# Optimization experiments

Hardware: AMD Instinct MI355X
Metric: run time of the kernel (lower is better)

## Reference

```python
import jax, jax.numpy as jnp
import numpy as np

KH, KW = 3, 3
PAD = 1
STRIDE = 1


def dht1(x):
    # 1D Discrete Hartley Transform along last axis: Re(FFT) - Im(FFT)
    f = jnp.fft.fft(x, axis=-1)
    return f.real - f.imag


def dht2(x, fft_h, fft_w):
    # zero-pad trailing two dims up to (fft_h, fft_w), then DHT along w then h
    pad_h = fft_h - x.shape[-2]
    pad_w = fft_w - x.shape[-1]
    pads = [(0, 0)] * (x.ndim - 2) + [(0, pad_h), (0, pad_w)]
    x = jnp.pad(x, pads)
    x = dht1(x)
    x = jnp.swapaxes(dht1(jnp.swapaxes(x, -1, -2)), -1, -2)
    return x


def setup_inputs() -> dict:
    key = jax.random.key(0)
    k1, k2 = jax.random.split(key)
    x = jax.random.normal(k1, (8, 64, 128, 128), dtype=jnp.float32)
    weight = jax.random.normal(k2, (64, 64, KH, KW), dtype=jnp.float32)
    return {"x": x, "weight": weight}


def reference(x, weight):
    b, c_in, h, w = x.shape
    out_h = (h + 2 * PAD - KH) // STRIDE + 1
    out_w = (w + 2 * PAD - KW) // STRIDE + 1
    x_p = jnp.pad(x, ((0, 0), (0, 0), (PAD, PAD), (PAD, PAD)))
    fft_h = h + 2 * PAD + KH - 1
    fft_w = w + 2 * PAD + KW - 1

    x_ht = dht2(x_p, fft_h, fft_w)          # [B, Cin, fh, fw]
    w_ht = dht2(weight, fft_h, fft_w)        # [Cout, Cin, fh, fw]

    x_f = jnp.flip(x_ht, axis=(-2, -1))
    w_f = jnp.flip(w_ht, axis=(-2, -1))

    # Fused combine + sum over Cin: avoids [B,Cout,Cin,fh,fw] intermediates.
    t1 = jnp.einsum('bchw,ochw->bohw', x_ht, w_ht)
    t2 = jnp.einsum('bchw,ochw->bohw', x_ht, w_f)
    t3 = jnp.einsum('bchw,ochw->bohw', x_f, w_ht)
    t4 = jnp.einsum('bchw,ochw->bohw', x_f, w_f)
    out_ht = (t1 + t2 + t3 - t4) * 0.5

    # idht2 in the source applies only the 1/n scaling twice (no transform)
    output = out_ht / jnp.asarray(fft_h * fft_w, dtype=out_ht.dtype)
    return output[:, :, :out_h, :out_w]
```

## Files before the change

kernel.cpp:

```cpp
#include <hip/hip_runtime.h>
#include <hip/hip_fp16.h>


#define SCALE (0.5f / 17424.0f)
#define MFMA  __builtin_amdgcn_mfma_f32_16x16x32_f16

typedef __attribute__((ext_vector_type(8))) _Float16 f16x8;
typedef __attribute__((ext_vector_type(4))) _Float16 f16x4;
typedef __attribute__((ext_vector_type(4))) float    f32x4;

__global__ __launch_bounds__(256) void build_all(
    const float* __restrict__ w, _Float16* __restrict__ Tf,
    _Float16* __restrict__ cfT, _Float16* __restrict__ hgT)
{
    const int bid = blockIdx.x;
    const int tid = threadIdx.x;
    const float step = 6.28318530717958647692f / 132.0f;
    if (bid < 144) {
        if (tid < 128) {
            float val = 0.f;
            if (bid < 132) {
                const int m = (bid * (tid + 1)) % 132;
                float s, c;
                sincosf((float)m * step, &s, &c);
                val = c + s;
            }
            Tf[bid * 128 + tid] = (_Float16)val;
        }
        return;
    }
    if (bid == 144) {
        if (tid < 128) {
            const int v = tid;
            float s, c;
            _Float16 o[8];
            o[0] = (_Float16)1.0f; o[3] = (_Float16)1.0f;
            o[6] = (_Float16)0.0f; o[7] = (_Float16)0.0f;
            sincosf((float)((v * 1) % 132) * step, &s, &c);       o[1] = (_Float16)(c + s);
            sincosf((float)((v * 2) % 132) * step, &s, &c);       o[2] = (_Float16)(c + s);
            sincosf((float)(((v + 1) * 1) % 132) * step, &s, &c); o[4] = (_Float16)(c - s);
            sincosf((float)(((v + 1) * 2) % 132) * step, &s, &c); o[5] = (_Float16)(c - s);
            *(f16x8*)(cfT + v * 8) = *(f16x8*)o;
        }
        return;
    }
    const int bid2 = bid - 145;
    const int u = bid2 >> 2;
    const int itbase = (bid2 & 3) * 4;
    float a[3], ap[3];
    a[0] = 1.f; ap[0] = 1.f;
    #pragma unroll
    for (int i = 1; i < 3; ++i) {
        float s, c;
        sincosf((float)((u * i) % 132) * step, &s, &c);
        a[i] = c + s;
        sincosf((float)(((u + 1) * i) % 132) * step, &s, &c);
        ap[i] = c - s;
    }
    for (int it = itbase; it < itbase + 4; ++it) {
        const int oc = it * 256 + tid;
        const float* wp = w + (size_t)oc * 9;
        float w9[9];
        #pragma unroll
        for (int q = 0; q < 9; ++q) w9[q] = wp[q];
        #pragma unroll
        for (int j = 0; j < 3; ++j) {
            const float h = a[0]*w9[j] + a[1]*w9[3+j] + a[2]*w9[6+j];
            const float g = ap[0]*w9[j] + ap[1]*w9[3+j] + ap[2]*w9[6+j];
            hgT[((size_t)u * 6 + j)     * 4096 + oc] = (_Float16)h;
            hgT[((size_t)u * 6 + 3 + j) * 4096 + oc] = (_Float16)g;
        }
    }
}

__global__ __launch_bounds__(512, 4) void dht2_fused(
    const float* __restrict__ x, const _Float16* __restrict__ Tf,
    _Float16* __restrict__ X)
{
    const int bc = blockIdx.x;
    const int tid = threadIdx.x, wv = tid >> 6, lane = tid & 63;
    const int col = lane & 15, quad = lane >> 4;
    __shared__ _Float16 Tfl[144][136];
    __shared__ _Float16 Y1l[144][136];

    const float* xp = x + (size_t)bc * 16384;
    const int ic = wv * 16 + col;

    float4 xv[4][2];
    #pragma unroll
    for (int kc = 0; kc < 4; ++kc) {
        const int k0 = kc * 32 + quad * 8;
        xv[kc][0] = *(const float4*)(xp + ic * 128 + k0);
        xv[kc][1] = *(const float4*)(xp + ic * 128 + k0 + 4);
    }
    #pragma unroll
    for (int s = 0; s < 5; ++s) {
        const int idx = tid + 512 * s;
        if (idx < 2304) {
            const int row = idx >> 4;
            const int ce  = (idx & 15) * 8;
            *(f16x8*)&Tfl[row][ce] = *(const f16x8*)(Tf + (size_t)idx * 8);
        }
    }
    f16x8 bfA[4];
    #pragma unroll
    for (int kc = 0; kc < 4; ++kc) {
        f16x8 t;
        t[0] = (_Float16)xv[kc][0].x; t[1] = (_Float16)xv[kc][0].y;
        t[2] = (_Float16)xv[kc][0].z; t[3] = (_Float16)xv[kc][0].w;
        t[4] = (_Float16)xv[kc][1].x; t[5] = (_Float16)xv[kc][1].y;
        t[6] = (_Float16)xv[kc][1].z; t[7] = (_Float16)xv[kc][1].w;
        bfA[kc] = t;
    }
    __syncthreads();

    f32x4 accA[9];
    #pragma unroll
    for (int mt = 0; mt < 9; ++mt) accA[mt] = (f32x4)0.f;
    #pragma unroll
    for (int kc = 0; kc < 4; ++kc) {
        const int k0 = kc * 32 + quad * 8;
        #pragma unroll
        for (int mt = 0; mt < 9; ++mt) {
            const f16x8 af = *(const f16x8*)&Tfl[mt * 16 + col][k0];
            accA[mt] = MFMA(af, bfA[kc], accA[mt], 0, 0, 0);
        }
    }
    #pragma unroll
    for (int mt = 0; mt < 9; ++mt)
        #pragma unroll
        for (int r = 0; r < 4; ++r)
            Y1l[mt * 16 + quad * 4 + r][ic] = (_Float16)accA[mt][r];
    __syncthreads();

    f32x4 accB[9];
    #pragma unroll
    for (int mt = 0; mt < 9; ++mt) accB[mt] = (f32x4)0.f;
    #pragma unroll
    for (int kc = 0; kc < 4; ++kc) {
        const int k0 = kc * 32 + quad * 8;
        const f16x8 bf = *(const f16x8*)&Y1l[wv * 16 + col][k0];
        #pragma unroll
        for (int mt = 0; mt < 9; ++mt) {
            const f16x8 af = *(const f16x8*)&Tfl[mt * 16 + col][k0];
            accB[mt] = MFMA(af, bf, accB[mt], 0, 0, 0);
        }
    }
    f32x4 accT[3];
    #pragma unroll
    for (int j = 0; j < 3; ++j) accT[j] = (f32x4)0.f;
    if (wv < 4) {
        #pragma unroll
        for (int kc = 0; kc < 4; ++kc) {
            const int k0 = kc * 32 + quad * 8;
            const f16x8 bf = *(const f16x8*)&Y1l[128 + col][k0];
            #pragma unroll
            for (int j = 0; j < 3; ++j) {
                if (j < 2 || wv == 0) {
                    const int mt = (j == 2) ? 8 : (wv * 2 + j);
                    const f16x8 af = *(const f16x8*)&Tfl[mt * 16 + col][k0];
                    accT[j] = MFMA(af, bf, accT[j], 0, 0, 0);
                }
            }
        }
    }
    __syncthreads();

    #pragma unroll
    for (int mt = 0; mt < 9; ++mt)
        #pragma unroll
        for (int r = 0; r < 4; ++r)
            Tfl[mt * 16 + quad * 4 + r][wv * 16 + col] = (_Float16)accB[mt][r];
    if (wv < 4 && col < 4) {
        #pragma unroll
        for (int j = 0; j < 3; ++j) {
            if (j < 2 || wv == 0) {
                const int mt = (j == 2) ? 8 : (wv * 2 + j);
                #pragma unroll
                for (int r = 0; r < 4; ++r)
                    Tfl[mt * 16 + quad * 4 + r][128 + col] = (_Float16)accT[j][r];
            }
        }
    }
    __syncthreads();
    _Float16* Xp = X + (size_t)bc * 17952;
    #pragma unroll
    for (int s = 0; s < 5; ++s) {
        const int ch = tid + 512 * s;
        if (ch < 2244) {
            const int u = ch / 17, kk = ch - u * 17;
            *(f16x8*)(Xp + u * 136 + kk * 8) = *(const f16x8*)&Tfl[u][kk * 8];
        }
    }
}

__global__ __launch_bounds__(512, 2) void combine_mfma(
    const _Float16* __restrict__ X, const _Float16* __restrict__ hgT,
    const _Float16* __restrict__ cfT, float* __restrict__ out)
{
    const int uidx = blockIdx.x;
    const int tid = threadIdx.x;
    const int wv8 = tid >> 6;
    const int half = wv8 >> 2;
    const int wv = wv8 & 3;
    const int lane = tid & 63;
    const int col = lane & 15, quad = lane >> 4;
    const int b = blockIdx.y * 2 + half;
    const int u2 = 131 - uidx;
    const bool doB = (uidx >= 4);

    __shared__ _Float16 Ps[2][132][72];
    __shared__ _Float16 Ms[2][132][72];

    {
        const int th = tid & 255;
        const int c = th >> 2, sub = th & 3;
        const _Float16* rowd = X + (size_t)(b * 64 + c) * 17952 + (size_t)uidx * 136;
        const _Float16* rowm = X + (size_t)(b * 64 + c) * 17952 + (size_t)u2 * 136;
        #pragma unroll
        for (int k = 0; k < 8; ++k) {
            const int v0 = sub * 32 + 4 * k;
            const f16x4 d = *(const f16x4*)(rowd + v0);
            const f16x4 m = *(const f16x4*)(rowm + (128 - v0));
            #pragma unroll
            for (int i = 0; i < 4; ++i) {
                Ps[half][v0 + i][c] = d[i] + m[3 - i];
                Ms[half][v0 + i][c] = d[i] - m[3 - i];
            }
        }
        if (sub == 0) {
            const f16x4 d = *(const f16x4*)(rowd + 128);
            const f16x4 m = *(const f16x4*)(rowm);
            #pragma unroll
            for (int i = 0; i < 4; ++i) {
                Ps[half][128 + i][c] = d[i] + m[3 - i];
                Ms[half][128 + i][c] = d[i] - m[3 - i];
            }
        }
    }

    const _Float16* hgu = hgT + (size_t)uidx * 6 * 4096;
    const int orow = wv * 16 + col;
    f16x8 hA[3][2], gA[3][2];
    #pragma unroll
    for (int kt = 0; kt < 3; ++kt)
        #pragma unroll
        for (int hf = 0; hf < 2; ++hf) {
            hA[kt][hf] = *(const f16x8*)(hgu + ((size_t)kt * 64 + orow) * 64 + hf * 32 + quad * 8);
            gA[kt][hf] = *(const f16x8*)(hgu + ((size_t)(3 + kt) * 64 + orow) * 64 + hf * 32 + quad * 8);
        }
    __syncthreads();

    float* outA = out + (((size_t)(b * 64 + wv * 16 + quad * 4)) * 128 + uidx) * 128 + col;
    float* outB = out + (((size_t)(b * 64 + wv * 16 + quad * 4)) * 128 + u2) * 128 + col;

    #pragma unroll
    for (int nt = 0; nt < 8; ++nt) {
        const int vA = nt * 16 + col;
        const int vB = 131 - vA;
        const f16x8 cf8 = *(const f16x8*)(cfT + (size_t)(nt * 16 + col) * 8);
        const float c1 = (float)cf8[1], c2 = (float)cf8[2];
        const float d1 = (float)cf8[4], d2 = (float)cf8[5];
        {
            const f16x8 p0 = *(const f16x8*)&Ps[half][vA][quad * 8];
            const f16x8 p1 = *(const f16x8*)&Ps[half][vA][32 + quad * 8];
            const f16x8 m0 = *(const f16x8*)&Ms[half][vA][quad * 8];
            const f16x8 m1 = *(const f16x8*)&Ms[half][vA][32 + quad * 8];
            f32x4 aP0 = (f32x4)0.f, aP1 = (f32x4)0.f, aP2 = (f32x4)0.f;
            f32x4 aM0 = (f32x4)0.f, aM1 = (f32x4)0.f, aM2 = (f32x4)0.f;
            aP0 = MFMA(hA[0][0], p0, aP0, 0, 0, 0); aP0 = MFMA(hA[0][1], p1, aP0, 0, 0, 0);
            aP1 = MFMA(hA[1][0], p0, aP1, 0, 0, 0); aP1 = MFMA(hA[1][1], p1, aP1, 0, 0, 0);
            aP2 = MFMA(hA[2][0], p0, aP2, 0, 0, 0); aP2 = MFMA(hA[2][1], p1, aP2, 0, 0, 0);
            aM0 = MFMA(gA[0][0], m0, aM0, 0, 0, 0); aM0 = MFMA(gA[0][1], m1, aM0, 0, 0, 0);
            aM1 = MFMA(gA[1][0], m0, aM1, 0, 0, 0); aM1 = MFMA(gA[1][1], m1, aM1, 0, 0, 0);
            aM2 = MFMA(gA[2][0], m0, aM2, 0, 0, 0); aM2 = MFMA(gA[2][1], m1, aM2, 0, 0, 0);
            #pragma unroll
            for (int r = 0; r < 4; ++r)
                outA[(size_t)r * 16384 + nt * 16] =
                    ((aP0[r] + c1 * aP1[r] + c2 * aP2[r]) +
                     (aM0[r] + d1 * aM1[r] + d2 * aM2[r])) * SCALE;
        }
        if (doB) {
            const f16x8 p0 = *(const f16x8*)&Ps[half][vB][quad * 8];
            const f16x8 p1 = *(const f16x8*)&Ps[half][vB][32 + quad * 8];
            const f16x8 m0 = *(const f16x8*)&Ms[half][vB][quad * 8];
            const f16x8 m1 = *(const f16x8*)&Ms[half][vB][32 + quad * 8];
            f32x4 bP0 = (f32x4)0.f, bP1 = (f32x4)0.f, bP2 = (f32x4)0.f;
            f32x4 bM0 = (f32x4)0.f, bM1 = (f32x4)0.f, bM2 = (f32x4)0.f;
            bP0 = MFMA(gA[0][0], p0, bP0, 0, 0, 0); bP0 = MFMA(gA[0][1], p1, bP0, 0, 0, 0);
            bP1 = MFMA(gA[1][0], p0, bP1, 0, 0, 0); bP1 = MFMA(gA[1][1], p1, bP1, 0, 0, 0);
            bP2 = MFMA(gA[2][0], p0, bP2, 0, 0, 0); bP2 = MFMA(gA[2][1], p1, bP2, 0, 0, 0);
            bM0 = MFMA(hA[0][0], m0, bM0, 0, 0, 0); bM0 = MFMA(hA[0][1], m1, bM0, 0, 0, 0);
            bM1 = MFMA(hA[1][0], m0, bM1, 0, 0, 0); bM1 = MFMA(hA[1][1], m1, bM1, 0, 0, 0);
            bM2 = MFMA(hA[2][0], m0, bM2, 0, 0, 0); bM2 = MFMA(hA[2][1], m1, bM2, 0, 0, 0);
            #pragma unroll
            for (int r = 0; r < 4; ++r)
                outB[(size_t)r * 16384 + nt * 16] =
                    ((bP0[r] + c1 * bP1[r] + c2 * bP2[r]) -
                     (bM0[r] + d1 * bM1[r] + d2 * bM2[r])) * SCALE;
        }
    }
}

extern "C" void kernel_launch(void* const* d_in, const int* in_sizes, int n_in,
                              void* d_out, int out_size, void* d_ws, size_t ws_size,
                              hipStream_t stream)
{
    const float* x = (const float*)d_in[0];
    const float* w = (const float*)d_in[1];
    char* ws = (char*)d_ws;
    _Float16* Tf  = (_Float16*)(ws);
    _Float16* cfT = (_Float16*)(ws + 36864);
    _Float16* X   = (_Float16*)(ws + 65536);
    _Float16* hgT = (_Float16*)(ws + 18448384);

    build_all<<<dim3(409), dim3(256), 0, stream>>>(w, Tf, cfT, hgT);

    dht2_fused<<<dim3(512), dim3(512), 0, stream>>>(x, Tf, X);

    combine_mfma<<<dim3(66, 4), dim3(512), 0, stream>>>(
        X, hgT, cfT, (float*)d_out);
}
```

Baseline: 115.5 us.

## Merge table-build and DHT kernels, compute twiddles in-block, shrink combine blocks

Folds the weight/cf preparation kernel into the DHT kernel as extra blocks, removing one launch and the global Tf table. Each DHT block now builds its 144x128 twiddle matrix in shared memory from a 132-entry sin+cos table rather than loading it from global memory. The combine kernel goes from 512-thread blocks covering two batches to 256-thread blocks covering one batch, doubling the grid. The trade-off is extra sincos and modulo work per DHT block, plus an added barrier.

```diff
diff --git a/kernel.cpp b/kernel.cpp
--- a/kernel.cpp
+++ b/kernel.cpp
@@ -9,79 +9,65 @@
 typedef __attribute__((ext_vector_type(4))) _Float16 f16x4;
 typedef __attribute__((ext_vector_type(4))) float    f32x4;
 
-__global__ __launch_bounds__(256) void build_all(
-    const float* __restrict__ w, _Float16* __restrict__ Tf,
-    _Float16* __restrict__ cfT, _Float16* __restrict__ hgT)
+__global__ __launch_bounds__(512, 4) void dht2_prep(
+    const float* __restrict__ x, const float* __restrict__ w,
+    _Float16* __restrict__ X, _Float16* __restrict__ cfT,
+    _Float16* __restrict__ hgT)
 {
-    const int bid = blockIdx.x;
     const int tid = threadIdx.x;
     const float step = 6.28318530717958647692f / 132.0f;
-    if (bid < 144) {
-        if (tid < 128) {
-            float val = 0.f;
-            if (bid < 132) {
-                const int m = (bid * (tid + 1)) % 132;
+
+    if (blockIdx.x >= 512) {
+        const int bid2 = blockIdx.x - 512;
+        if (bid2 == 66) {
+            if (tid < 128) {
+                const int v = tid;
                 float s, c;
-                sincosf((float)m * step, &s, &c);
-                val = c + s;
-            }
-            Tf[bid * 128 + tid] = (_Float16)val;
+                _Float16 o[8];
+                o[0] = (_Float16)1.0f; o[3] = (_Float16)1.0f;
+                o[6] = (_Float16)0.0f; o[7] = (_Float16)0.0f;
+                sincosf((float)((v * 1) % 132) * step, &s, &c);       o[1] = (_Float16)(c + s);
+                sincosf((float)((v * 2) % 132) * step, &s, &c);       o[2] = (_Float16)(c + s);
+                sincosf((float)(((v + 1) * 1) % 132) * step, &s, &c); o[4] = (_Float16)(c - s);
+                sincosf((float)(((v + 1) * 2) % 132) * step, &s, &c); o[5] = (_Float16)(c - s);
+                *(f16x8*)(cfT + v * 8) = *(f16x8*)o;
+            }
+            return;
+        }
+        const int u = bid2;
+        float a[3], ap[3];
+        a[0] = 1.f; ap[0] = 1.f;
+        #pragma unroll
+        for (int i = 1; i < 3; ++i) {
+            float s, c;
+            sincosf((float)((u * i) % 132) * step, &s, &c);
+            a[i] = c + s;
+            sincosf((float)(((u + 1) * i) % 132) * step, &s, &c);
+            ap[i] = c - s;
+        }
+        for (int it = 0; it < 8; ++it) {
+            const int oc = it * 512 + tid;
+            const float* wp = w + (size_t)oc * 9;
+            float w9[9];
+            #pragma unroll
+            for (int q = 0; q < 9; ++q) w9[q] = wp[q];
+            #pragma unroll
+            for (int j = 0; j < 3; ++j) {
+                const float h = a[0]*w9[j] + a[1]*w9[3+j] + a[2]*w9[6+j];
+                const float g = ap[0]*w9[j] + ap[1]*w9[3+j] + ap[2]*w9[6+j];
+                hgT[((size_t)u * 6 + j)     * 4096 + oc] = (_Float16)h;
+                hgT[((size_t)u * 6 + 3 + j) * 4096 + oc] = (_Float16)g;
+            }
         }
         return;
     }
-    if (bid == 144) {
-        if (tid < 128) {
-            const int v = tid;
-            float s, c;
-            _Float16 o[8];
-            o[0] = (_Float16)1.0f; o[3] = (_Float16)1.0f;
-            o[6] = (_Float16)0.0f; o[7] = (_Float16)0.0f;
-            sincosf((float)((v * 1) % 132) * step, &s, &c);       o[1] = (_Float16)(c + s);
-            sincosf((float)((v * 2) % 132) * step, &s, &c);       o[2] = (_Float16)(c + s);
-            sincosf((float)(((v + 1) * 1) % 132) * step, &s, &c); o[4] = (_Float16)(c - s);
-            sincosf((float)(((v + 1) * 2) % 132) * step, &s, &c); o[5] = (_Float16)(c - s);
-            *(f16x8*)(cfT + v * 8) = *(f16x8*)o;
-        }
-        return;
-    }
-    const int bid2 = bid - 145;
-    const int u = bid2 >> 2;
-    const int itbase = (bid2 & 3) * 4;
-    float a[3], ap[3];
-    a[0] = 1.f; ap[0] = 1.f;
-    #pragma unroll
-    for (int i = 1; i < 3; ++i) {
-        float s, c;
-        sincosf((float)((u * i) % 132) * step, &s, &c);
-        a[i] = c + s;
-        sincosf((float)(((u + 1) * i) % 132) * step, &s, &c);
-        ap[i] = c - s;
-    }
-    for (int it = itbase; it < itbase + 4; ++it) {
-        const int oc = it * 256 + tid;
-        const float* wp = w + (size_t)oc * 9;
-        float w9[9];
-        #pragma unroll
-        for (int q = 0; q < 9; ++q) w9[q] = wp[q];
-        #pragma unroll
-        for (int j = 0; j < 3; ++j) {
-            const float h = a[0]*w9[j] + a[1]*w9[3+j] + a[2]*w9[6+j];
-            const float g = ap[0]*w9[j] + ap[1]*w9[3+j] + ap[2]*w9[6+j];
-            hgT[((size_t)u * 6 + j)     * 4096 + oc] = (_Float16)h;
-            hgT[((size_t)u * 6 + 3 + j) * 4096 + oc] = (_Float16)g;
-        }
-    }
-}
-
-__global__ __launch_bounds__(512, 4) void dht2_fused(
-    const float* __restrict__ x, const _Float16* __restrict__ Tf,
-    _Float16* __restrict__ X)
-{
+
     const int bc = blockIdx.x;
-    const int tid = threadIdx.x, wv = tid >> 6, lane = tid & 63;
+    const int wv = tid >> 6, lane = tid & 63;
     const int col = lane & 15, quad = lane >> 4;
     __shared__ _Float16 Tfl[144][136];
     __shared__ _Float16 Y1l[144][136];
+    __shared__ float castab[132];
 
     const float* xp = x + (size_t)bc * 16384;
     const int ic = wv * 16 + col;
@@ -93,14 +79,20 @@
         xv[kc][0] = *(const float4*)(xp + ic * 128 + k0);
         xv[kc][1] = *(const float4*)(xp + ic * 128 + k0 + 4);
     }
-    #pragma unroll
-    for (int s = 0; s < 5; ++s) {
-        const int idx = tid + 512 * s;
-        if (idx < 2304) {
-            const int row = idx >> 4;
-            const int ce  = (idx & 15) * 8;
-            *(f16x8*)&Tfl[row][ce] = *(const f16x8*)(Tf + (size_t)idx * 8);
-        }
+    if (tid < 132) {
+        float s, c;
+        sincosf((float)tid * step, &s, &c);
+        castab[tid] = c + s;
+    }
+    __syncthreads();
+    #pragma unroll
+    for (int s = 0; s < 36; ++s) {
+        const int idx = s * 512 + tid;
+        const int row = idx >> 7;
+        const int ci  = idx & 127;
+        float v = 0.f;
+        if (row < 132) v = castab[(row * (ci + 1)) % 132];
+        Tfl[row][ci] = (_Float16)v;
     }
     f16x8 bfA[4];
     #pragma unroll
@@ -194,27 +186,23 @@
     }
 }
 
-__global__ __launch_bounds__(512, 2) void combine_mfma(
+__global__ __launch_bounds__(256, 2) void combine_mfma(
     const _Float16* __restrict__ X, const _Float16* __restrict__ hgT,
     const _Float16* __restrict__ cfT, float* __restrict__ out)
 {
     const int uidx = blockIdx.x;
+    const int b = blockIdx.y;
     const int tid = threadIdx.x;
-    const int wv8 = tid >> 6;
-    const int half = wv8 >> 2;
-    const int wv = wv8 & 3;
-    const int lane = tid & 63;
+    const int wv = tid >> 6, lane = tid & 63;
     const int col = lane & 15, quad = lane >> 4;
-    const int b = blockIdx.y * 2 + half;
     const int u2 = 131 - uidx;
     const bool doB = (uidx >= 4);
 
-    __shared__ _Float16 Ps[2][132][72];
-    __shared__ _Float16 Ms[2][132][72];
+    __shared__ _Float16 Ps[132][72];
+    __shared__ _Float16 Ms[132][72];
 
     {
-        const int th = tid & 255;
-        const int c = th >> 2, sub = th & 3;
+        const int c = tid >> 2, sub = tid & 3;
         const _Float16* rowd = X + (size_t)(b * 64 + c) * 17952 + (size_t)uidx * 136;
         const _Float16* rowm = X + (size_t)(b * 64 + c) * 17952 + (size_t)u2 * 136;
         #pragma unroll
@@ -224,8 +212,8 @@
             const f16x4 m = *(const f16x4*)(rowm + (128 - v0));
             #pragma unroll
             for (int i = 0; i < 4; ++i) {
-                Ps[half][v0 + i][c] = d[i] + m[3 - i];
-                Ms[half][v0 + i][c] = d[i] - m[3 - i];
+                Ps[v0 + i][c] = d[i] + m[3 - i];
+                Ms[v0 + i][c] = d[i] - m[3 - i];
             }
         }
         if (sub == 0) {
@@ -233,8 +221,8 @@
             const f16x4 m = *(const f16x4*)(rowm);
             #pragma unroll
             for (int i = 0; i < 4; ++i) {
-                Ps[half][128 + i][c] = d[i] + m[3 - i];
-                Ms[half][128 + i][c] = d[i] - m[3 - i];
+                Ps[128 + i][c] = d[i] + m[3 - i];
+                Ms[128 + i][c] = d[i] - m[3 - i];
             }
         }
     }
@@ -262,10 +250,10 @@
         const float c1 = (float)cf8[1], c2 = (float)cf8[2];
         const float d1 = (float)cf8[4], d2 = (float)cf8[5];
         {
-            const f16x8 p0 = *(const f16x8*)&Ps[half][vA][quad * 8];
-            const f16x8 p1 = *(const f16x8*)&Ps[half][vA][32 + quad * 8];
-            const f16x8 m0 = *(const f16x8*)&Ms[half][vA][quad * 8];
-            const f16x8 m1 = *(const f16x8*)&Ms[half][vA][32 + quad * 8];
+            const f16x8 p0 = *(const f16x8*)&Ps[vA][quad * 8];
+            const f16x8 p1 = *(const f16x8*)&Ps[vA][32 + quad * 8];
+            const f16x8 m0 = *(const f16x8*)&Ms[vA][quad * 8];
+            const f16x8 m1 = *(const f16x8*)&Ms[vA][32 + quad * 8];
             f32x4 aP0 = (f32x4)0.f, aP1 = (f32x4)0.f, aP2 = (f32x4)0.f;
             f32x4 aM0 = (f32x4)0.f, aM1 = (f32x4)0.f, aM2 = (f32x4)0.f;
             aP0 = MFMA(hA[0][0], p0, aP0, 0, 0, 0); aP0 = MFMA(hA[0][1], p1, aP0, 0, 0, 0);
@@ -281,10 +269,10 @@
                      (aM0[r] + d1 * aM1[r] + d2 * aM2[r])) * SCALE;
         }
         if (doB) {
-            const f16x8 p0 = *(const f16x8*)&Ps[half][vB][quad * 8];
-            const f16x8 p1 = *(const f16x8*)&Ps[half][vB][32 + quad * 8];
-            const f16x8 m0 = *(const f16x8*)&Ms[half][vB][quad * 8];
-            const f16x8 m1 = *(const f16x8*)&Ms[half][vB][32 + quad * 8];
+            const f16x8 p0 = *(const f16x8*)&Ps[vB][quad * 8];
+            const f16x8 p1 = *(const f16x8*)&Ps[vB][32 + quad * 8];
+            const f16x8 m0 = *(const f16x8*)&Ms[vB][quad * 8];
+            const f16x8 m1 = *(const f16x8*)&Ms[vB][32 + quad * 8];
             f32x4 bP0 = (f32x4)0.f, bP1 = (f32x4)0.f, bP2 = (f32x4)0.f;
             f32x4 bM0 = (f32x4)0.f, bM1 = (f32x4)0.f, bM2 = (f32x4)0.f;
             bP0 = MFMA(gA[0][0], p0, bP0, 0, 0, 0); bP0 = MFMA(gA[0][1], p1, bP0, 0, 0, 0);
@@ -309,15 +297,12 @@
     const float* x = (const float*)d_in[0];
     const float* w = (const float*)d_in[1];
     char* ws = (char*)d_ws;
-    _Float16* Tf  = (_Float16*)(ws);
     _Float16* cfT = (_Float16*)(ws + 36864);
     _Float16* X   = (_Float16*)(ws + 65536);
     _Float16* hgT = (_Float16*)(ws + 18448384);
 
-    build_all<<<dim3(409), dim3(256), 0, stream>>>(w, Tf, cfT, hgT);
-
-    dht2_fused<<<dim3(512), dim3(512), 0, stream>>>(x, Tf, X);
-
-    combine_mfma<<<dim3(66, 4), dim3(512), 0, stream>>>(
+    dht2_prep<<<dim3(579), dim3(512), 0, stream>>>(x, w, X, cfT, hgT);
+
+    combine_mfma<<<dim3(66, 8), dim3(256), 0, stream>>>(
         X, hgT, cfT, (float*)d_out);
 }
```

After: 110.7 us. 4.2% less time.
